# Optimization experiments

Measured on AMD Instinct MI355X. Metric: run time of the kernel, lower is better.

## Reference

```python
import jax, jax.numpy as jnp
import numpy as np

HASHCODE_LEN = 8   # config.attention_hashcode_len (tau)
NUM_HEAD = 12      # config.num_attention_heads
KERNEL = 9         # config.attention_conv_kernel_size
B, H, S, D = 2, 12, 2048, 64


def _l2_normalize(x, eps=1e-12):
    # yoso.normalize: L2-normalize along last (head_dim) axis
    return x / jnp.maximum(jnp.linalg.norm(x, axis=-1, keepdims=True), eps)


def setup_inputs() -> dict:
    key = jax.random.key(0)
    kq, kk, kv, kw = jax.random.split(key, 4)
    Q = jax.random.normal(kq, (B, H, S, D), jnp.float32)
    K = jax.random.normal(kk, (B, H, S, D), jnp.float32)
    V = jax.random.normal(kv, (B, H, S, D), jnp.float32)
    mask = jnp.ones((B, S), jnp.float32)
    conv_w = jax.random.normal(kw, (H, 1, KERNEL, 1), jnp.float32) * 0.02
    return {"Q": Q, "K": K, "V": V, "mask": mask, "conv_w": conv_w}


def reference(Q, K, V, mask, conv_w):
    # conv skip path: depthwise (groups=num_head) Conv2d over the seq axis of masked V
    Vm = V * mask[:, None, :, None]                       # [B,H,S,D]
    conv_V = jax.lax.conv_general_dilated(
        Vm, conv_w, window_strides=(1, 1),
        padding=((KERNEL // 2, KERNEL // 2), (0, 0)),
        dimension_numbers=("NCHW", "OIHW", "NCHW"),
        feature_group_count=H)

    # yoso_e exact-expectation branch (num_hash_f < 0): normalize Q, K, then
    # attention weight = E[hash collision] = (1 - arccos(q.k)/pi)^hashcode_len
    Qn = _l2_normalize(Q)
    Kn = _l2_normalize(K)
    qk = jnp.einsum("bhsd,bhtd->bhst", Qn, Kn)            # [B,H,S,S]
    qk = jnp.clip(qk, -1.0 + 1e-6, 1.0 - 1e-6)            # keep arccos grad finite
    w = (1.0 - jnp.arccos(qk) / jnp.pi) ** HASHCODE_LEN
    w = w * mask[:, None, None, :]                        # key-side mask
    X = jnp.einsum("bhst,bhtd->bhsd", w, V)
    X = X * mask[:, None, :, None]                        # query-side mask
    X = _l2_normalize(X)                                  # yoso.normalize(X)
    return X + conv_V
```

## Files before the change

kernel.cpp:

```cpp
#include <hip/hip_runtime.h>
#include <hip/hip_bf16.h>
#include <math.h>

typedef __attribute__((ext_vector_type(4))) float f32x4;
typedef __attribute__((ext_vector_type(8))) short bf16x8;
typedef __attribute__((ext_vector_type(4))) int i32x4;

#define NB 2
#define NH 12
#define NS 2048
#define ND 64
#define NKER 9
#define BH (NB*NH)
#define BHS (NB*NH*NS)
#define NT (NS/64)

using bf16 = __hip_bfloat16;

__device__ __forceinline__ f32x4 mfma16x16x32_bf16(bf16x8 a, bf16x8 b, f32x4 c) {
  return __builtin_amdgcn_mfma_f32_16x16x32_bf16(a, b, c, 0, 0, 0);
}

__global__ void normalize_qk(const float* __restrict__ Q, const float* __restrict__ K,
                             bf16* __restrict__ Qn, bf16* __restrict__ Kn) {
  int wid  = (blockIdx.x * blockDim.x + threadIdx.x) >> 6;
  int lane = threadIdx.x & 63;
  if (wid >= 2 * BHS) return;
  const float* src; bf16* dst; int row;
  if (wid < BHS) { src = Q; dst = Qn; row = wid; }
  else           { src = K; dst = Kn; row = wid - BHS; }
  float v  = src[(size_t)row * ND + lane];
  float ss = v * v;
  #pragma unroll
  for (int m = 1; m < 64; m <<= 1) ss += __shfl_xor(ss, m);
  float scale = 1.0f / fmaxf(sqrtf(ss), 1e-12f);
  dst[(size_t)row * ND + lane] = __float2bfloat16(v * scale);
}

__global__ __launch_bounds__(256) void conv_vt(
    const float* __restrict__ V, const float* __restrict__ mask,
    const float* __restrict__ cw, float* __restrict__ out, bf16* __restrict__ Vmt) {
  __shared__ float tile[72][68];
  __shared__ float wsm[NKER];
  int bh = blockIdx.y, b = bh / NH, h = bh % NH;
  int s0 = blockIdx.x * 64;
  int tid = threadIdx.x;
  if (tid < NKER) wsm[tid] = cw[h * NKER + tid];

  int r  = tid >> 2;
  int c0 = (tid & 3) * 16;
  #pragma unroll
  for (int pass = 0; pass < 2; ++pass) {
    int rr = r + pass * 64;
    if (pass == 0 || tid < 32) {
      int gs = s0 - NKER / 2 + rr;
      bool ok = (gs >= 0 && gs < NS);
      float m = ok ? mask[b * NS + gs] : 0.f;
      #pragma unroll
      for (int j = 0; j < 16; ++j)
        tile[rr][c0 + j] = ok ? V[((size_t)bh * NS + gs) * ND + c0 + j] * m : 0.f;
    }
  }
  __syncthreads();

  {
    int s = tid >> 2;
    float acc[16];
    #pragma unroll
    for (int j = 0; j < 16; ++j) acc[j] = 0.f;
    #pragma unroll
    for (int k = 0; k < NKER; ++k) {
      float w = wsm[k];
      #pragma unroll
      for (int j = 0; j < 16; ++j) acc[j] += tile[s + k][c0 + j] * w;
    }
    float* dst = out + ((size_t)bh * NS + s0 + s) * ND + c0;
    #pragma unroll
    for (int j = 0; j < 16; ++j) dst[j] = acc[j];
  }
  {
    int d = tid >> 2;
    bf16* dst = Vmt + (size_t)bh * ND * NS + (size_t)d * NS + s0 + c0;
    #pragma unroll
    for (int j = 0; j < 16; ++j)
      dst[j] = __float2bfloat16(tile[NKER / 2 + c0 + j][d]);
  }
}

__global__ __launch_bounds__(512) void yoso_attn(
    const bf16* __restrict__ Qn, const bf16* __restrict__ Kn,
    const bf16* __restrict__ Vmt, const float* __restrict__ mask,
    float* __restrict__ out) {
  __shared__ __align__(16) char lds[48 * 1024];

  int tid  = threadIdx.x;
  int wave = tid >> 6;
  int lane = tid & 63;
  int lo   = lane & 15;
  int hi   = lane >> 4;
  int qsub = wave >> 1;
  int kh   = wave & 1;
  int bh   = blockIdx.y;
  int b    = bh / NH;
  int q0   = blockIdx.x * 64;

  const bf16* Qbh = Qn  + (size_t)bh * NS * ND;
  const bf16* Kbh = Kn  + (size_t)bh * NS * ND;
  const bf16* Vbh = Vmt + (size_t)bh * ND * NS;

  int qrow = q0 + qsub * 16 + lo;
  bf16x8 aq0 = *(const bf16x8*)(Qbh + (size_t)qrow * ND + hi * 8);
  bf16x8 aq1 = *(const bf16x8*)(Qbh + (size_t)qrow * ND + 32 + hi * 8);

  f32x4 xacc[4];
  #pragma unroll
  for (int i = 0; i < 4; ++i) xacc[i] = (f32x4){0.f, 0.f, 0.f, 0.f};

  int row0 = tid >> 3, coff0 = (tid & 7) * 16;
  int dst0 = row0 * 128 + (coff0 ^ ((row0 & 7) << 4));
  const char* Ks0 = (const char*)(Kbh + (size_t)row0 * ND) + coff0;
  const char* Vs0 = (const char*)(Vbh + (size_t)row0 * NS) + coff0;

  *(i32x4*)(lds + dst0)        = *(const i32x4*)Ks0;
  *(i32x4*)(lds + 8192 + dst0) = *(const i32x4*)Vs0;

  char* pw = lds + 32768 + wave * 2048;
  i32x4 kr, vr;

  for (int kt = 0; kt < NT; ++kt) {
    __syncthreads();
    if (kt < NT - 1) {
      kr = *(const i32x4*)(Ks0 + (size_t)(kt + 1) * 8192);
      vr = *(const i32x4*)(Vs0 + (size_t)(kt + 1) * 128);
    }
    char* kb = lds + (kt & 1) * 16384;
    char* vb = kb + 8192;

    #pragma unroll
    for (int cgl = 0; cgl < 2; ++cgl) {
      int cg   = kh * 2 + cgl;
      f32x4 s  = (f32x4){0.f, 0.f, 0.f, 0.f};
      int krow = cg * 16 + lo;
      const char* kbase = kb + krow * 128;
      int sw = (krow & 7) << 4;
      bf16x8 bk0 = *(const bf16x8*)(kbase + ((hi * 16) ^ sw));
      bf16x8 bk1 = *(const bf16x8*)(kbase + ((64 + hi * 16) ^ sw));
      s = mfma16x16x32_bf16(aq0, bk0, s);
      s = mfma16x16x32_bf16(aq1, bk1, s);
      #pragma unroll
      for (int r = 0; r < 4; ++r) {
        float x = s[r];
        float a = fminf(fabsf(x), 0.999999f);
        float sq = __builtin_amdgcn_sqrtf(1.0f - a);
        float p = fmaf(fmaf(fmaf(-0.005961377f, a, 0.02363857f), a,
                            -0.06751758f), a, 0.49998939f);
        float u = sq * p;
        float t = (x >= 0.0f) ? (1.0f - u) : u;
        float t2 = t * t, t4 = t2 * t2, w = t4 * t4;
        int prow = hi * 4 + r;
        int pcol = cgl * 16 + lo;
        *(bf16*)(pw + prow * 128 + ((pcol * 2) ^ ((prow & 7) << 4))) = __float2bfloat16(w);
      }
    }

    {
      const char* pbase = pw + lo * 128;
      bf16x8 ap = *(const bf16x8*)(pbase + ((hi * 16) ^ ((lo & 7) << 4)));
      #pragma unroll
      for (int dg = 0; dg < 4; ++dg) {
        int drow = dg * 16 + lo;
        const char* vbase = vb + drow * 128;
        bf16x8 bv = *(const bf16x8*)(vbase + ((kh * 64 + hi * 16) ^ ((drow & 7) << 4)));
        xacc[dg] = mfma16x16x32_bf16(ap, bv, xacc[dg]);
      }
    }

    if (kt < NT - 1) {
      char* kbn = lds + ((kt + 1) & 1) * 16384;
      *(i32x4*)(kbn + dst0)        = kr;
      *(i32x4*)(kbn + 8192 + dst0) = vr;
    }
  }

  __syncthreads();
  float* cmb = (float*)(lds + 32768);
  if (kh == 1) {
    #pragma unroll
    for (int r = 0; r < 4; ++r)
      #pragma unroll
      for (int dg = 0; dg < 4; ++dg)
        cmb[qsub * 1024 + (hi * 4 + r) * 64 + dg * 16 + lo] = xacc[dg][r];
  }
  __syncthreads();
  if (kh == 0) {
    #pragma unroll
    for (int r = 0; r < 4; ++r) {
      int row = q0 + qsub * 16 + hi * 4 + r;
      float m = mask[b * NS + row];
      float vals[4];
      float ss = 0.f;
      #pragma unroll
      for (int dg = 0; dg < 4; ++dg) {
        float x = (xacc[dg][r] + cmb[qsub * 1024 + (hi * 4 + r) * 64 + dg * 16 + lo]) * m;
        vals[dg] = x;
        ss += x * x;
      }
      #pragma unroll
      for (int mm = 1; mm < 16; mm <<= 1) ss += __shfl_xor(ss, mm);
      float scale = 1.0f / fmaxf(sqrtf(ss), 1e-12f);
      size_t base = ((size_t)bh * NS + row) * ND;
      #pragma unroll
      for (int dg = 0; dg < 4; ++dg)
        out[base + dg * 16 + lo] += vals[dg] * scale;
    }
  }
}

extern "C" void kernel_launch(void* const* d_in, const int* in_sizes, int n_in,
                              void* d_out, int out_size, void* d_ws, size_t ws_size,
                              hipStream_t stream) {
  const float* Q    = (const float*)d_in[0];
  const float* K    = (const float*)d_in[1];
  const float* V    = (const float*)d_in[2];
  const float* mask = (const float*)d_in[3];
  const float* cw   = (const float*)d_in[4];
  float* out = (float*)d_out;

  bf16* Qn  = (bf16*)d_ws;
  bf16* Kn  = Qn + (size_t)BHS * ND;
  bf16* Vmt = Kn + (size_t)BHS * ND;

  normalize_qk<<<2 * BHS / 4, 256, 0, stream>>>(Q, K, Qn, Kn);
  conv_vt<<<dim3(NS / 64, BH), 256, 0, stream>>>(V, mask, cw, out, Vmt);
  yoso_attn<<<dim3(NS / 64, BH), 512, 0, stream>>>(Qn, Kn, Vmt, mask, out);
}
```

Before: 93.27 us.

## Switch attention to 32x32x16 MFMA, fuse K-normalize into prep, normalize Q in-kernel

Replaces the 16x16x32 MFMA tiles with 32x32x16 bf16 MFMA, so each wave handles 32 queries by 32 keys, and the block shrinks to 4 waves. K normalization moves into the conv/transpose prep kernel and Q normalization into the attention kernel, which drops one launch and the Qn round trip through memory. Stores become vectorized with a manual bf16 round-to-nearest-even. Fewer waves per block and larger per-wave register use could reduce occupancy.

```diff
diff --git a/kernel.cpp b/kernel.cpp
--- a/kernel.cpp
+++ b/kernel.cpp
@@ -2,9 +2,10 @@
 #include <hip/hip_bf16.h>
 #include <math.h>
 
-typedef __attribute__((ext_vector_type(4))) float f32x4;
-typedef __attribute__((ext_vector_type(8))) short bf16x8;
-typedef __attribute__((ext_vector_type(4))) int i32x4;
+typedef __attribute__((ext_vector_type(4)))  float f32x4;
+typedef __attribute__((ext_vector_type(16))) float f32x16;
+typedef __attribute__((ext_vector_type(8)))  short bf16x8;
+typedef __attribute__((ext_vector_type(4)))  int   i32x4;
 
 #define NB 2
 #define NH 12
@@ -17,29 +18,20 @@
 
 using bf16 = __hip_bfloat16;
 
-__device__ __forceinline__ f32x4 mfma16x16x32_bf16(bf16x8 a, bf16x8 b, f32x4 c) {
-  return __builtin_amdgcn_mfma_f32_16x16x32_bf16(a, b, c, 0, 0, 0);
-}
-
-__global__ void normalize_qk(const float* __restrict__ Q, const float* __restrict__ K,
-                             bf16* __restrict__ Qn, bf16* __restrict__ Kn) {
-  int wid  = (blockIdx.x * blockDim.x + threadIdx.x) >> 6;
-  int lane = threadIdx.x & 63;
-  if (wid >= 2 * BHS) return;
-  const float* src; bf16* dst; int row;
-  if (wid < BHS) { src = Q; dst = Qn; row = wid; }
-  else           { src = K; dst = Kn; row = wid - BHS; }
-  float v  = src[(size_t)row * ND + lane];
-  float ss = v * v;
-  #pragma unroll
-  for (int m = 1; m < 64; m <<= 1) ss += __shfl_xor(ss, m);
-  float scale = 1.0f / fmaxf(sqrtf(ss), 1e-12f);
-  dst[(size_t)row * ND + lane] = __float2bfloat16(v * scale);
-}
-
-__global__ __launch_bounds__(256) void conv_vt(
-    const float* __restrict__ V, const float* __restrict__ mask,
-    const float* __restrict__ cw, float* __restrict__ out, bf16* __restrict__ Vmt) {
+__device__ __forceinline__ f32x16 mfma32(bf16x8 a, bf16x8 b, f32x16 c) {
+  return __builtin_amdgcn_mfma_f32_32x32x16_bf16(a, b, c, 0, 0, 0);
+}
+
+__device__ __forceinline__ unsigned short bf16rne(float f) {
+  unsigned u = __builtin_bit_cast(unsigned, f);
+  u += 0x7FFFu + ((u >> 16) & 1u);
+  return (unsigned short)(u >> 16);
+}
+
+__global__ __launch_bounds__(256) void prep(
+    const float* __restrict__ K, const float* __restrict__ V,
+    const float* __restrict__ mask, const float* __restrict__ cw,
+    float* __restrict__ out, bf16* __restrict__ Kn, bf16* __restrict__ Vmt) {
   __shared__ float tile[72][68];
   __shared__ float wsm[NKER];
   int bh = blockIdx.y, b = bh / NH, h = bh % NH;
@@ -49,6 +41,24 @@
 
   int r  = tid >> 2;
   int c0 = (tid & 3) * 16;
+
+  {
+    const float* Kr = K + ((size_t)bh * NS + s0 + r) * ND + c0;
+    float v[16]; float ss = 0.f;
+    #pragma unroll
+    for (int j = 0; j < 16; ++j) { v[j] = Kr[j]; ss += v[j] * v[j]; }
+    ss += __shfl_xor(ss, 1); ss += __shfl_xor(ss, 2);
+    float sc = rsqrtf(fmaxf(ss, 1e-24f));
+    bf16x8 o0, o1;
+    #pragma unroll
+    for (int j = 0; j < 8; ++j) {
+      o0[j] = (short)bf16rne(v[j] * sc);
+      o1[j] = (short)bf16rne(v[8 + j] * sc);
+    }
+    bf16* dst = Kn + ((size_t)bh * NS + s0 + r) * ND + c0;
+    *(bf16x8*)dst = o0; *(bf16x8*)(dst + 8) = o1;
+  }
+
   #pragma unroll
   for (int pass = 0; pass < 2; ++pass) {
     int rr = r + pass * 64;
@@ -64,7 +74,6 @@
   __syncthreads();
 
   {
-    int s = tid >> 2;
     float acc[16];
     #pragma unroll
     for (int j = 0; j < 16; ++j) acc[j] = 0.f;
@@ -72,146 +81,185 @@
     for (int k = 0; k < NKER; ++k) {
       float w = wsm[k];
       #pragma unroll
-      for (int j = 0; j < 16; ++j) acc[j] += tile[s + k][c0 + j] * w;
-    }
-    float* dst = out + ((size_t)bh * NS + s0 + s) * ND + c0;
+      for (int j = 0; j < 16; ++j) acc[j] += tile[r + k][c0 + j] * w;
+    }
+    float* dst = out + ((size_t)bh * NS + s0 + r) * ND + c0;
     #pragma unroll
     for (int j = 0; j < 16; ++j) dst[j] = acc[j];
   }
   {
-    int d = tid >> 2;
-    bf16* dst = Vmt + (size_t)bh * ND * NS + (size_t)d * NS + s0 + c0;
-    #pragma unroll
-    for (int j = 0; j < 16; ++j)
-      dst[j] = __float2bfloat16(tile[NKER / 2 + c0 + j][d]);
-  }
-}
-
-__global__ __launch_bounds__(512) void yoso_attn(
-    const bf16* __restrict__ Qn, const bf16* __restrict__ Kn,
+    bf16x8 o0, o1;
+    #pragma unroll
+    for (int j = 0; j < 8; ++j) {
+      o0[j] = (short)bf16rne(tile[NKER / 2 + c0 + j][r]);
+      o1[j] = (short)bf16rne(tile[NKER / 2 + c0 + 8 + j][r]);
+    }
+    bf16* dst = Vmt + (size_t)bh * ND * NS + (size_t)r * NS + s0 + c0;
+    *(bf16x8*)dst = o0; *(bf16x8*)(dst + 8) = o1;
+  }
+}
+
+__global__ __launch_bounds__(256) void yoso_attn(
+    const float* __restrict__ Q, const bf16* __restrict__ Kn,
     const bf16* __restrict__ Vmt, const float* __restrict__ mask,
     float* __restrict__ out) {
-  __shared__ __align__(16) char lds[48 * 1024];
+  __shared__ __align__(16) char lds[40 * 1024];
 
   int tid  = threadIdx.x;
   int wave = tid >> 6;
   int lane = tid & 63;
-  int lo   = lane & 15;
-  int hi   = lane >> 4;
+  int ql   = lane & 31;
+  int c    = lane >> 5;
   int qsub = wave >> 1;
   int kh   = wave & 1;
   int bh   = blockIdx.y;
   int b    = bh / NH;
   int q0   = blockIdx.x * 64;
 
-  const bf16* Qbh = Qn  + (size_t)bh * NS * ND;
   const bf16* Kbh = Kn  + (size_t)bh * NS * ND;
   const bf16* Vbh = Vmt + (size_t)bh * ND * NS;
 
-  int qrow = q0 + qsub * 16 + lo;
-  bf16x8 aq0 = *(const bf16x8*)(Qbh + (size_t)qrow * ND + hi * 8);
-  bf16x8 aq1 = *(const bf16x8*)(Qbh + (size_t)qrow * ND + 32 + hi * 8);
-
-  f32x4 xacc[4];
-  #pragma unroll
-  for (int i = 0; i < 4; ++i) xacc[i] = (f32x4){0.f, 0.f, 0.f, 0.f};
-
-  int row0 = tid >> 3, coff0 = (tid & 7) * 16;
-  int dst0 = row0 * 128 + (coff0 ^ ((row0 & 7) << 4));
-  const char* Ks0 = (const char*)(Kbh + (size_t)row0 * ND) + coff0;
-  const char* Vs0 = (const char*)(Vbh + (size_t)row0 * NS) + coff0;
-
-  *(i32x4*)(lds + dst0)        = *(const i32x4*)Ks0;
-  *(i32x4*)(lds + 8192 + dst0) = *(const i32x4*)Vs0;
+  bf16x8 aq[4];
+  {
+    int qrow = q0 + qsub * 32 + ql;
+    const float* Qr = Q + ((size_t)bh * NS + qrow) * ND;
+    float qv[32]; float ss = 0.f;
+    #pragma unroll
+    for (int t = 0; t < 4; ++t) {
+      f32x4 a0 = *(const f32x4*)(Qr + t * 16 + c * 8);
+      f32x4 a1 = *(const f32x4*)(Qr + t * 16 + c * 8 + 4);
+      #pragma unroll
+      for (int j = 0; j < 4; ++j) {
+        qv[t * 8 + j] = a0[j]; qv[t * 8 + 4 + j] = a1[j];
+        ss += a0[j] * a0[j] + a1[j] * a1[j];
+      }
+    }
+    ss += __shfl_xor(ss, 32);
+    float sc = rsqrtf(fmaxf(ss, 1e-24f));
+    #pragma unroll
+    for (int t = 0; t < 4; ++t)
+      #pragma unroll
+      for (int j = 0; j < 8; ++j)
+        aq[t][j] = (short)bf16rne(qv[t * 8 + j] * sc);
+  }
+
+  f32x16 xacc[2] = {};
+
+  int srow = tid >> 3;
+  int scol = (tid & 7) * 16;
+  int sw   = (srow & 7) << 4;
+  int d0 = srow * 128 + (scol ^ sw);
+  int d1 = (srow + 32) * 128 + (scol ^ sw);
+  const char* KsA = (const char*)Kbh + (size_t)srow * 128 + scol;
+  const char* KsB = (const char*)Kbh + (size_t)(srow + 32) * 128 + scol;
+  const char* VsA = (const char*)Vbh + (size_t)srow * (NS * 2) + scol;
+  const char* VsB = (const char*)Vbh + (size_t)(srow + 32) * (NS * 2) + scol;
+
+  *(i32x4*)(lds + d0)        = *(const i32x4*)KsA;
+  *(i32x4*)(lds + d1)        = *(const i32x4*)KsB;
+  *(i32x4*)(lds + 8192 + d0) = *(const i32x4*)VsA;
+  *(i32x4*)(lds + 8192 + d1) = *(const i32x4*)VsB;
+
+  int krow = kh * 32 + ql;
+  int ksw  = (krow & 7) << 4;
+  int kboff[4];
+  #pragma unroll
+  for (int t = 0; t < 4; ++t) kboff[t] = krow * 128 + ((t * 32 + c * 16) ^ ksw);
+  int pslot_r = ((ql >> 2) & 3) << 4;
+  int poff[2];
+  #pragma unroll
+  for (int ks = 0; ks < 2; ++ks) poff[ks] = ql * 64 + ((ks * 32 + c * 16) ^ pslot_r);
+  int bvoff[2][2];
+  #pragma unroll
+  for (int dt = 0; dt < 2; ++dt) {
+    int drow = dt * 32 + ql;
+    int vsw  = (drow & 7) << 4;
+    #pragma unroll
+    for (int ks = 0; ks < 2; ++ks)
+      bvoff[dt][ks] = drow * 128 + ((kh * 64 + ks * 32 + c * 16) ^ vsw);
+  }
 
   char* pw = lds + 32768 + wave * 2048;
-  i32x4 kr, vr;
+  i32x4 kA, kB, vA, vB;
 
   for (int kt = 0; kt < NT; ++kt) {
     __syncthreads();
     if (kt < NT - 1) {
-      kr = *(const i32x4*)(Ks0 + (size_t)(kt + 1) * 8192);
-      vr = *(const i32x4*)(Vs0 + (size_t)(kt + 1) * 128);
+      kA = *(const i32x4*)(KsA + (size_t)(kt + 1) * 8192);
+      kB = *(const i32x4*)(KsB + (size_t)(kt + 1) * 8192);
+      vA = *(const i32x4*)(VsA + (size_t)(kt + 1) * 128);
+      vB = *(const i32x4*)(VsB + (size_t)(kt + 1) * 128);
     }
     char* kb = lds + (kt & 1) * 16384;
     char* vb = kb + 8192;
 
-    #pragma unroll
-    for (int cgl = 0; cgl < 2; ++cgl) {
-      int cg   = kh * 2 + cgl;
-      f32x4 s  = (f32x4){0.f, 0.f, 0.f, 0.f};
-      int krow = cg * 16 + lo;
-      const char* kbase = kb + krow * 128;
-      int sw = (krow & 7) << 4;
-      bf16x8 bk0 = *(const bf16x8*)(kbase + ((hi * 16) ^ sw));
-      bf16x8 bk1 = *(const bf16x8*)(kbase + ((64 + hi * 16) ^ sw));
-      s = mfma16x16x32_bf16(aq0, bk0, s);
-      s = mfma16x16x32_bf16(aq1, bk1, s);
-      #pragma unroll
-      for (int r = 0; r < 4; ++r) {
-        float x = s[r];
-        float a = fminf(fabsf(x), 0.999999f);
-        float sq = __builtin_amdgcn_sqrtf(1.0f - a);
-        float p = fmaf(fmaf(fmaf(-0.005961377f, a, 0.02363857f), a,
-                            -0.06751758f), a, 0.49998939f);
-        float u = sq * p;
-        float t = (x >= 0.0f) ? (1.0f - u) : u;
-        float t2 = t * t, t4 = t2 * t2, w = t4 * t4;
-        int prow = hi * 4 + r;
-        int pcol = cgl * 16 + lo;
-        *(bf16*)(pw + prow * 128 + ((pcol * 2) ^ ((prow & 7) << 4))) = __float2bfloat16(w);
+    f32x16 s{};
+    #pragma unroll
+    for (int t = 0; t < 4; ++t) {
+      bf16x8 bk = *(const bf16x8*)(kb + kboff[t]);
+      s = mfma32(aq[t], bk, s);
+    }
+
+    #pragma unroll
+    for (int r = 0; r < 16; ++r) {
+      float x  = s[r];
+      float a  = fminf(fabsf(x), 0.999999f);
+      float sq = __builtin_amdgcn_sqrtf(1.0f - a);
+      float p  = fmaf(fmaf(fmaf(-0.005961377f, a, 0.02363857f), a,
+                           -0.06751758f), a, 0.49998939f);
+      float u  = sq * p;
+      float t1 = (x >= 0.0f) ? (1.0f - u) : u;
+      float t2 = t1 * t1, t4 = t2 * t2, w = t4 * t4;
+      int q_loc = (r & 3) + 8 * (r >> 2) + 4 * c;
+      *(short*)(pw + q_loc * 64 + ((ql * 2) ^ ((((q_loc >> 2) & 3)) << 4))) =
+          (short)bf16rne(w);
+    }
+
+    #pragma unroll
+    for (int ks = 0; ks < 2; ++ks) {
+      bf16x8 ap = *(const bf16x8*)(pw + poff[ks]);
+      #pragma unroll
+      for (int dt = 0; dt < 2; ++dt) {
+        bf16x8 bv = *(const bf16x8*)(vb + bvoff[dt][ks]);
+        xacc[dt] = mfma32(ap, bv, xacc[dt]);
       }
     }
 
-    {
-      const char* pbase = pw + lo * 128;
-      bf16x8 ap = *(const bf16x8*)(pbase + ((hi * 16) ^ ((lo & 7) << 4)));
-      #pragma unroll
-      for (int dg = 0; dg < 4; ++dg) {
-        int drow = dg * 16 + lo;
-        const char* vbase = vb + drow * 128;
-        bf16x8 bv = *(const bf16x8*)(vbase + ((kh * 64 + hi * 16) ^ ((drow & 7) << 4)));
-        xacc[dg] = mfma16x16x32_bf16(ap, bv, xacc[dg]);
+    if (kt < NT - 1) {
+      char* nb = lds + ((kt + 1) & 1) * 16384;
+      *(i32x4*)(nb + d0)        = kA;
+      *(i32x4*)(nb + d1)        = kB;
+      *(i32x4*)(nb + 8192 + d0) = vA;
+      *(i32x4*)(nb + 8192 + d1) = vB;
+    }
+  }
+
+  float* cmb = (float*)lds;
+  if (kh == 1) {
+    #pragma unroll
+    for (int dt = 0; dt < 2; ++dt)
+      #pragma unroll
+      for (int r = 0; r < 16; ++r) {
+        int q_loc = (r & 3) + 8 * (r >> 2) + 4 * c;
+        cmb[qsub * 2048 + q_loc * 64 + dt * 32 + ql] = xacc[dt][r];
       }
-    }
-
-    if (kt < NT - 1) {
-      char* kbn = lds + ((kt + 1) & 1) * 16384;
-      *(i32x4*)(kbn + dst0)        = kr;
-      *(i32x4*)(kbn + 8192 + dst0) = vr;
-    }
-  }
-
-  __syncthreads();
-  float* cmb = (float*)(lds + 32768);
-  if (kh == 1) {
-    #pragma unroll
-    for (int r = 0; r < 4; ++r)
-      #pragma unroll
-      for (int dg = 0; dg < 4; ++dg)
-        cmb[qsub * 1024 + (hi * 4 + r) * 64 + dg * 16 + lo] = xacc[dg][r];
   }
   __syncthreads();
   if (kh == 0) {
     #pragma unroll
-    for (int r = 0; r < 4; ++r) {
-      int row = q0 + qsub * 16 + hi * 4 + r;
+    for (int r = 0; r < 16; ++r) {
+      int q_loc = (r & 3) + 8 * (r >> 2) + 4 * c;
+      int row = q0 + qsub * 32 + q_loc;
       float m = mask[b * NS + row];
-      float vals[4];
-      float ss = 0.f;
-      #pragma unroll
-      for (int dg = 0; dg < 4; ++dg) {
-        float x = (xacc[dg][r] + cmb[qsub * 1024 + (hi * 4 + r) * 64 + dg * 16 + lo]) * m;
-        vals[dg] = x;
-        ss += x * x;
-      }
-      #pragma unroll
-      for (int mm = 1; mm < 16; mm <<= 1) ss += __shfl_xor(ss, mm);
-      float scale = 1.0f / fmaxf(sqrtf(ss), 1e-12f);
+      float x0 = (xacc[0][r] + cmb[qsub * 2048 + q_loc * 64 + ql]) * m;
+      float x1 = (xacc[1][r] + cmb[qsub * 2048 + q_loc * 64 + 32 + ql]) * m;
+      float s2 = x0 * x0 + x1 * x1;
+      #pragma unroll
+      for (int mm = 1; mm < 32; mm <<= 1) s2 += __shfl_xor(s2, mm);
+      float sc = rsqrtf(fmaxf(s2, 1e-24f));
       size_t base = ((size_t)bh * NS + row) * ND;
-      #pragma unroll
-      for (int dg = 0; dg < 4; ++dg)
-        out[base + dg * 16 + lo] += vals[dg] * scale;
+      out[base + ql]      += x0 * sc;
+      out[base + 32 + ql] += x1 * sc;
     }
   }
 }
@@ -226,11 +274,9 @@
   const float* cw   = (const float*)d_in[4];
   float* out = (float*)d_out;
 
-  bf16* Qn  = (bf16*)d_ws;
-  bf16* Kn  = Qn + (size_t)BHS * ND;
+  bf16* Kn  = (bf16*)d_ws;
   bf16* Vmt = Kn + (size_t)BHS * ND;
 
-  normalize_qk<<<2 * BHS / 4, 256, 0, stream>>>(Q, K, Qn, Kn);
-  conv_vt<<<dim3(NS / 64, BH), 256, 0, stream>>>(V, mask, cw, out, Vmt);
-  yoso_attn<<<dim3(NS / 64, BH), 512, 0, stream>>>(Qn, Kn, Vmt, mask, out);
-}
+  prep<<<dim3(NS / 64, BH), 256, 0, stream>>>(K, V, mask, cw, out, Kn, Vmt);
+  yoso_attn<<<dim3(NS / 64, BH), 256, 0, stream>>>(Q, Kn, Vmt, mask, out);
+}
```

Measured after the change: 89.54 us. -4.0%, faster.
